# Performance work log

Hardware: AMD Instinct MI355X
Metric: run time of the kernel (lower is better)

## Reference

```python
import jax, jax.numpy as jnp
import numpy as np

NEG_SLOPE = 0.2  # leaky_relu_negative_slope


def setup_inputs() -> dict:
    key = jax.random.key(0)
    k = jax.random.split(key, 6)
    N = 1024          # n_nodes == nei_nodes (forced by the asserts in forward)
    IN = 256          # in_features
    OUT = 256         # out_features (nei_embedding feature dim, since linear_r = Linear(out_features, ...))
    H, F = 4, 64      # n_heads, n_hidden = out_features // n_heads
    h = jax.random.normal(k[0], (N, IN), dtype=jnp.float32)
    nei_embedding = jax.random.normal(k[1], (N, OUT), dtype=jnp.float32)
    adj_mat = jax.random.randint(k[2], (N, N), 0, 2).astype(jnp.float32)
    scale = 0.05
    w_l = jax.random.normal(k[3], (IN, H * F), dtype=jnp.float32) * scale   # linear_l.weight.T
    w_r = jax.random.normal(k[4], (OUT, H * F), dtype=jnp.float32) * scale  # linear_r.weight.T
    attn_w = jax.random.normal(k[5], (F,), dtype=jnp.float32) * scale       # attn.weight (1, F) -> (F,)
    return {"h": h, "nei_embedding": nei_embedding, "adj_mat": adj_mat,
            "w_l": w_l, "w_r": w_r, "attn_w": attn_w, "use_elu": 1}


def reference(h, nei_embedding, adj_mat, w_l, w_r, attn_w, use_elu):
    N = h.shape[0]
    M = nei_embedding.shape[0]
    F = attn_w.shape[0]
    H = w_l.shape[1] // F
    g_l = (h @ w_l).reshape(N, H, F)              # (N, H, F)
    g_r = (nei_embedding @ w_r).reshape(M, H, F)  # (M, H, F)
    # Torch does repeat/repeat_interleave then view(n, m, H, F); with the
    # assert-enforced n == m this is exactly g_sum[i, j] = g_l[j] + g_r[i].
    g_sum = g_r[:, None, :, :] + g_l[None, :, :, :]          # (N, N, H, F)
    e = jnp.einsum("nmhf,f->nmh", jax.nn.leaky_relu(g_sum, NEG_SLOPE), attn_w)
    adj_t = adj_mat.T[:, :, None]                             # (M, N, 1) -> broadcasts over heads
    e = jnp.where(adj_t == 0, -jnp.inf, e)
    exp_attention = jnp.exp(e)
    weighted = exp_attention * adj_t                          # (N, N, H)
    denom = jnp.sum(weighted, axis=1, keepdims=True)
    a = weighted / denom                                      # masked softmax over neighbors
    # dropout is identity at inference
    attn_res = jnp.einsum("ijh,jhf->ihf", a, g_r)            # (N, H, F)
    if use_elu:
        attn_res = jax.nn.elu(attn_res)
    return attn_res.reshape(N, H * F)  # is_concat=True
```

## Files before the change

### kernel.cpp

```cpp
#include <hip/hip_runtime.h>
#include <math.h>

#define NN 1024
#define KK 256
#define NH 4
#define FD 64
#define HF 256

__global__ __launch_bounds__(256) void gatv2_gemm(
    const float* __restrict__ h, const float* __restrict__ nei,
    const float* __restrict__ w_l, const float* __restrict__ w_r,
    float* __restrict__ g_l, float* __restrict__ g_r)
{
    const float* A; const float* W; float* G;
    if (blockIdx.z == 0) { A = h;   W = w_l; G = g_l; }
    else                 { A = nei; W = w_r; G = g_r; }

    __shared__ float sA[16][68];
    __shared__ float sW[16][64];

    const int t   = threadIdx.x;
    const int tm4 = (t >> 4) << 2;
    const int tn4 = (t & 15) << 2;
    const int m0  = blockIdx.y * 64;
    const int n0  = blockIdx.x * 64;

    float acc[4][4] = {};

    const int ar = t >> 2, ac = (t & 3) << 2;
    const int wr = t >> 4, wc = (t & 15) << 2;

    for (int k0 = 0; k0 < KK; k0 += 16) {
        float4 va = *(const float4*)&A[(size_t)(m0 + ar)*KK + k0 + ac];
        float4 vw = *(const float4*)&W[(size_t)(k0 + wr)*HF + n0 + wc];
        __syncthreads();
        sA[ac+0][ar] = va.x; sA[ac+1][ar] = va.y;
        sA[ac+2][ar] = va.z; sA[ac+3][ar] = va.w;
        *(float4*)&sW[wr][wc] = vw;
        __syncthreads();
        #pragma unroll
        for (int kk = 0; kk < 16; ++kk) {
            float4 a4 = *(const float4*)&sA[kk][tm4];
            float4 w4 = *(const float4*)&sW[kk][tn4];
            const float am[4] = {a4.x, a4.y, a4.z, a4.w};
            const float wn[4] = {w4.x, w4.y, w4.z, w4.w};
            #pragma unroll
            for (int mi = 0; mi < 4; ++mi)
                #pragma unroll
                for (int ni = 0; ni < 4; ++ni)
                    acc[mi][ni] += am[mi] * wn[ni];
        }
    }
    #pragma unroll
    for (int mi = 0; mi < 4; ++mi)
        *(float4*)&G[(size_t)(m0 + tm4 + mi)*HF + n0 + tn4] =
            make_float4(acc[mi][0], acc[mi][1], acc[mi][2], acc[mi][3]);
}

__global__ __launch_bounds__(256) void gatv2_cl(
    const float* __restrict__ g_l, const float* __restrict__ aw, float* __restrict__ cl)
{
    const int idx = blockIdx.x*256 + threadIdx.x;
    const int j = idx >> 2, hh = idx & 3;
    const float4* row = (const float4*)(g_l + (size_t)j*HF + hh*FD);
    const float4* wp  = (const float4*)aw;
    float s = 0.f;
    #pragma unroll
    for (int q = 0; q < 16; ++q) {
        float4 g = row[q], w = wp[q];
        s += g.x*w.x + g.y*w.y + g.z*w.z + g.w*w.w;
    }
    cl[idx] = 0.6f * s;
}

__global__ __launch_bounds__(256, 2) void gatv2_attn(
    const float* __restrict__ g_l, const float* __restrict__ g_r,
    const float* __restrict__ adj, const float* __restrict__ attn_w,
    const float* __restrict__ cl,
    float* __restrict__ accP, float* __restrict__ denP, int JPB)
{
    const int t  = threadIdx.x;
    const int jc = blockIdx.x;
    const int ib = blockIdx.y;
    const int hh = blockIdx.z;
    const int i  = ib*256 + t;

    const float4* wp = (const float4*)attn_w;

    float4 gri[16];
    float crdot = 0.f;
    {
        const float4* gp = (const float4*)(g_r + (size_t)i*HF + hh*FD);
        #pragma unroll
        for (int q = 0; q < 16; ++q) {
            float4 g = gp[q], w = wp[q];
            gri[q] = g;
            crdot += w.x*g.x + w.y*g.y + w.z*g.z + w.w*g.w;
        }
    }
    const float cr = 0.6f * crdot;

    float4 acc[16];
    #pragma unroll
    for (int q = 0; q < 16; ++q) acc[q] = make_float4(0.f,0.f,0.f,0.f);
    float denom = 0.f;

    const int jbase = jc * JPB;
    const float* glh = g_l + (size_t)hh*FD;
    const float* grh = g_r + (size_t)hh*FD;

    float mask_next = adj[(size_t)jbase*NN + i];
    for (int jj = 0; jj < JPB; ++jj) {
        const int j = jbase + jj;
        const float mask = mask_next;
        if (jj + 1 < JPB) mask_next = adj[(size_t)(j + 1)*NN + i];
        const float clj = cl[j*NH + hh];
        const float4* glr = (const float4*)(glh + (size_t)j*HF);
        float e0 = 0.f, e1 = 0.f, e2 = 0.f, e3 = 0.f;
        #pragma unroll
        for (int q = 0; q < 16; ++q) {
            float4 g = glr[q], w = wp[q];
            e0 += w.x * fabsf(g.x + gri[q].x);
            e1 += w.y * fabsf(g.y + gri[q].y);
            e2 += w.z * fabsf(g.z + gri[q].z);
            e3 += w.w * fabsf(g.w + gri[q].w);
        }
        const float e = cr + clj + 0.4f * ((e0+e1) + (e2+e3));
        const float pw = (mask != 0.f) ? __expf(e) : 0.f;
        denom += pw;
        const float4* grr = (const float4*)(grh + (size_t)j*HF);
        #pragma unroll
        for (int q = 0; q < 16; ++q) {
            float4 g = grr[q];
            acc[q].x += pw*g.x; acc[q].y += pw*g.y;
            acc[q].z += pw*g.z; acc[q].w += pw*g.w;
        }
    }
    float* op = accP + (size_t)jc*(NN*HF) + ((size_t)i*NH + hh)*FD;
    #pragma unroll
    for (int q = 0; q < 16; ++q) ((float4*)op)[q] = acc[q];
    denP[(size_t)jc*(NN*NH) + (size_t)i*NH + hh] = denom;
}

__global__ __launch_bounds__(256) void gatv2_reduce(
    const float* __restrict__ accP, const float* __restrict__ denP,
    const int* __restrict__ use_elu, float* __restrict__ out, int NC)
{
    const int idx = blockIdx.x*256 + threadIdx.x;
    float s = 0.f, d = 0.f;
    for (int c = 0; c < NC; ++c) {
        s += accP[(size_t)c*(NN*HF) + idx];
        d += denP[(size_t)c*(NN*NH) + (idx >> 6)];
    }
    float r = s / d;
    if (*use_elu != 0) r = (r > 0.f) ? r : expm1f(r);
    out[idx] = r;
}

extern "C" void kernel_launch(void* const* d_in, const int* in_sizes, int n_in,
                              void* d_out, int out_size, void* d_ws, size_t ws_size,
                              hipStream_t stream)
{
    const float* h    = (const float*)d_in[0];
    const float* nei  = (const float*)d_in[1];
    const float* adj  = (const float*)d_in[2];
    const float* w_l  = (const float*)d_in[3];
    const float* w_r  = (const float*)d_in[4];
    const float* aw   = (const float*)d_in[5];
    const int*   uel  = (const int*)d_in[6];
    float* out = (float*)d_out;
    float* ws  = (float*)d_ws;

    float* g_l = ws;
    float* g_r = g_l + (size_t)NN*HF;
    float* cl  = g_r + (size_t)NN*HF;

    int NC = 32;
    while (NC > 1) {
        size_t need = ((size_t)2*NN*HF + (size_t)NN*NH
                     + (size_t)NC*NN*NH + (size_t)NC*NN*HF) * sizeof(float);
        if (need <= ws_size) break;
        NC >>= 1;
    }
    const int JPB = NN / NC;

    float* denP = cl + (size_t)NN*NH;
    float* accP = denP + (size_t)NC*NN*NH;

    hipLaunchKernelGGL(gatv2_gemm, dim3(HF/64, NN/64, 2), dim3(256), 0, stream,
                       h, nei, w_l, w_r, g_l, g_r);
    hipLaunchKernelGGL(gatv2_cl, dim3((NN*NH)/256), dim3(256), 0, stream,
                       g_l, aw, cl);
    hipLaunchKernelGGL(gatv2_attn, dim3(NC, NN/256, NH), dim3(256), 0, stream,
                       g_l, g_r, adj, aw, cl, accP, denP, JPB);
    hipLaunchKernelGGL(gatv2_reduce, dim3((NN*HF)/256), dim3(256), 0, stream,
                       accP, denP, uel, out, NC);
}
```

Baseline: 171.0 us.

## Split attention into score kernel with scalar loads and separate PV kernel

Replaces the single fused attention kernel with a score kernel that writes the full masked exp matrix P to workspace, and a separate P·g_r accumulation kernel. The score kernel loads wave-uniform g_l rows through scalar loads in inline asm. The GEMM now computes the cl/cr attention dot products in its epilogue with atomics, which removes the separate cl kernel. Denominators are accumulated atomically after a memset. The aim is to cut redundant vector loads and register pressure in the attention loop, at the cost of a 16MB intermediate P round-trip through memory, an extra memset, and float atomics that make summation order nondeterministic.

```diff
diff --git a/kernel.cpp b/kernel.cpp
--- a/kernel.cpp
+++ b/kernel.cpp
@@ -7,152 +7,206 @@
 #define FD 64
 #define HF 256
 
+typedef __attribute__((ext_vector_type(16))) float fx16;
+
+#define OFF_GL   0
+#define OFF_GR   (256*1024)
+#define OFF_CL   (512*1024)
+#define OFF_CR   (512*1024 + 4096)
+#define OFF_DEN  (512*1024 + 8192)
+#define OFF_P    (512*1024 + 12288)
+#define OFF_ACCP (OFF_P + 4*1024*1024)
+
 __global__ __launch_bounds__(256) void gatv2_gemm(
-    const float* __restrict__ h, const float* __restrict__ nei,
+    const float* __restrict__ hmat, const float* __restrict__ nei,
     const float* __restrict__ w_l, const float* __restrict__ w_r,
-    float* __restrict__ g_l, float* __restrict__ g_r)
-{
-    const float* A; const float* W; float* G;
-    if (blockIdx.z == 0) { A = h;   W = w_l; G = g_l; }
-    else                 { A = nei; W = w_r; G = g_r; }
-
-    __shared__ float sA[16][68];
-    __shared__ float sW[16][64];
-
-    const int t   = threadIdx.x;
-    const int tm4 = (t >> 4) << 2;
-    const int tn4 = (t & 15) << 2;
-    const int m0  = blockIdx.y * 64;
-    const int n0  = blockIdx.x * 64;
-
-    float acc[4][4] = {};
-
-    const int ar = t >> 2, ac = (t & 3) << 2;
-    const int wr = t >> 4, wc = (t & 15) << 2;
-
-    for (int k0 = 0; k0 < KK; k0 += 16) {
-        float4 va = *(const float4*)&A[(size_t)(m0 + ar)*KK + k0 + ac];
-        float4 vw = *(const float4*)&W[(size_t)(k0 + wr)*HF + n0 + wc];
-        __syncthreads();
-        sA[ac+0][ar] = va.x; sA[ac+1][ar] = va.y;
-        sA[ac+2][ar] = va.z; sA[ac+3][ar] = va.w;
-        *(float4*)&sW[wr][wc] = vw;
-        __syncthreads();
+    const float* __restrict__ aw, float* __restrict__ ws)
+{
+    __shared__ float sA[64*257];
+    const int t  = threadIdx.x;
+    const int mb = blockIdx.x;
+    const int hh = blockIdx.y;
+    const int mat = blockIdx.z;
+    const float* A = mat ? nei : hmat;
+    const float* W = mat ? w_r : w_l;
+    float* G  = ws + (mat ? OFF_GR : OFF_GL);
+    float* CC = ws + (mat ? OFF_CR : OFF_CL);
+
+    const int lane = t & 63;
+    const int wv   = t >> 6;
+    const int m    = mb*64 + lane;
+    const int n0   = hh*64 + wv*16;
+
+    #pragma unroll
+    for (int rep = 0; rep < 16; ++rep) {
+        const int flat = rep*1024 + t*4;
+        const int r = flat >> 8, c = flat & 255;
+        *(float4*)&sA[r*257 + c] = *(const float4*)&A[(size_t)(mb*64 + r)*KK + c];
+    }
+    __syncthreads();
+
+    float acc[16] = {};
+    const float* wp = W + n0;
+    #pragma unroll 4
+    for (int k = 0; k < KK; ++k) {
+        const float a = sA[lane*257 + k];
+        const float4 w0 = *(const float4*)(wp + (size_t)k*HF);
+        const float4 w1 = *(const float4*)(wp + (size_t)k*HF + 4);
+        const float4 w2 = *(const float4*)(wp + (size_t)k*HF + 8);
+        const float4 w3 = *(const float4*)(wp + (size_t)k*HF + 12);
+        acc[0]  += a*w0.x; acc[1]  += a*w0.y; acc[2]  += a*w0.z; acc[3]  += a*w0.w;
+        acc[4]  += a*w1.x; acc[5]  += a*w1.y; acc[6]  += a*w1.z; acc[7]  += a*w1.w;
+        acc[8]  += a*w2.x; acc[9]  += a*w2.y; acc[10] += a*w2.z; acc[11] += a*w2.w;
+        acc[12] += a*w3.x; acc[13] += a*w3.y; acc[14] += a*w3.z; acc[15] += a*w3.w;
+    }
+
+    {
+        const float4* awp = (const float4*)(aw + wv*16);
+        float wd = 0.f;
         #pragma unroll
-        for (int kk = 0; kk < 16; ++kk) {
-            float4 a4 = *(const float4*)&sA[kk][tm4];
-            float4 w4 = *(const float4*)&sW[kk][tn4];
-            const float am[4] = {a4.x, a4.y, a4.z, a4.w};
-            const float wn[4] = {w4.x, w4.y, w4.z, w4.w};
-            #pragma unroll
-            for (int mi = 0; mi < 4; ++mi)
-                #pragma unroll
-                for (int ni = 0; ni < 4; ++ni)
-                    acc[mi][ni] += am[mi] * wn[ni];
+        for (int c = 0; c < 4; ++c) {
+            const float4 w4 = awp[c];
+            wd += w4.x*acc[c*4] + w4.y*acc[c*4+1] + w4.z*acc[c*4+2] + w4.w*acc[c*4+3];
         }
-    }
-    #pragma unroll
-    for (int mi = 0; mi < 4; ++mi)
-        *(float4*)&G[(size_t)(m0 + tm4 + mi)*HF + n0 + tn4] =
-            make_float4(acc[mi][0], acc[mi][1], acc[mi][2], acc[mi][3]);
-}
-
-__global__ __launch_bounds__(256) void gatv2_cl(
-    const float* __restrict__ g_l, const float* __restrict__ aw, float* __restrict__ cl)
-{
-    const int idx = blockIdx.x*256 + threadIdx.x;
-    const int j = idx >> 2, hh = idx & 3;
-    const float4* row = (const float4*)(g_l + (size_t)j*HF + hh*FD);
-    const float4* wp  = (const float4*)aw;
-    float s = 0.f;
-    #pragma unroll
-    for (int q = 0; q < 16; ++q) {
-        float4 g = row[q], w = wp[q];
-        s += g.x*w.x + g.y*w.y + g.z*w.z + g.w*w.w;
-    }
-    cl[idx] = 0.6f * s;
-}
-
-__global__ __launch_bounds__(256, 2) void gatv2_attn(
-    const float* __restrict__ g_l, const float* __restrict__ g_r,
-    const float* __restrict__ adj, const float* __restrict__ attn_w,
-    const float* __restrict__ cl,
-    float* __restrict__ accP, float* __restrict__ denP, int JPB)
-{
+        atomicAdd(&CC[hh*NN + m], 0.6f*wd);
+    }
+
+    __syncthreads();
+    #pragma unroll
+    for (int c = 0; c < 4; ++c)
+        *(float4*)&sA[lane*65 + wv*16 + c*4] =
+            make_float4(acc[c*4], acc[c*4+1], acc[c*4+2], acc[c*4+3]);
+    __syncthreads();
+    #pragma unroll
+    for (int rep = 0; rep < 4; ++rep) {
+        const int flat = rep*1024 + t*4;
+        const int ml = flat >> 6, f = flat & 63;
+        const float4 v = *(const float4*)&sA[ml*65 + f];
+        *(float4*)&G[(size_t)(mb*64 + ml)*HF + hh*64 + f] = v;
+    }
+}
+
+#define EBLK(RV, QB)                                              \
+    { _Pragma("unroll") for (int q = 0; q < 4; ++q) {             \
+        const float4 wq = w[(QB)+q]; const float4 gq = gri[(QB)+q]; \
+        e0 += wq.x * fabsf(RV[q*4+0] + gq.x);                     \
+        e1 += wq.y * fabsf(RV[q*4+1] + gq.y);                     \
+        e2 += wq.z * fabsf(RV[q*4+2] + gq.z);                     \
+        e3 += wq.w * fabsf(RV[q*4+3] + gq.w); } }
+
+__global__ __launch_bounds__(256, 3) void gatv2_e(
+    const float* __restrict__ wsro, const float* __restrict__ adj,
+    const float* __restrict__ aw, float* __restrict__ P,
+    float* __restrict__ den)
+{
+    const float* g_l = wsro + OFF_GL;
+    const float* g_r = wsro + OFF_GR;
+    const float* cl  = wsro + OFF_CL;
+    const float* cr  = wsro + OFF_CR;
     const int t  = threadIdx.x;
     const int jc = blockIdx.x;
     const int ib = blockIdx.y;
     const int hh = blockIdx.z;
     const int i  = ib*256 + t;
 
-    const float4* wp = (const float4*)attn_w;
-
-    float4 gri[16];
-    float crdot = 0.f;
+    float4 w[16], gri[16];
     {
-        const float4* gp = (const float4*)(g_r + (size_t)i*HF + hh*FD);
+        const float4* awp = (const float4*)aw;
+        const float4* gp  = (const float4*)(g_r + (size_t)i*HF + hh*FD);
         #pragma unroll
-        for (int q = 0; q < 16; ++q) {
-            float4 g = gp[q], w = wp[q];
-            gri[q] = g;
-            crdot += w.x*g.x + w.y*g.y + w.z*g.z + w.w*g.w;
-        }
-    }
-    const float cr = 0.6f * crdot;
-
-    float4 acc[16];
-    #pragma unroll
-    for (int q = 0; q < 16; ++q) acc[q] = make_float4(0.f,0.f,0.f,0.f);
-    float denom = 0.f;
-
-    const int jbase = jc * JPB;
-    const float* glh = g_l + (size_t)hh*FD;
-    const float* grh = g_r + (size_t)hh*FD;
-
-    float mask_next = adj[(size_t)jbase*NN + i];
+        for (int q = 0; q < 16; ++q) { w[q] = awp[q]; gri[q] = gp[q]; }
+    }
+    const float cri = cr[hh*NN + i];
+
+    float denl = 0.f;
+    const int j0 = jc*32;
+    for (int jj = 0; jj < 32; ++jj) {
+        const int j = j0 + jj;
+        const float mask = adj[(size_t)j*NN + i];
+        fx16 r0, r1, r2, r3; float clv;
+        const float* rowp = g_l + (size_t)j*HF + hh*FD;
+        const float* clp  = cl + hh*NN + j;
+        asm volatile(
+            "s_load_dwordx16 %0, %5, 0x0\n\t"
+            "s_load_dwordx16 %1, %5, 0x40\n\t"
+            "s_load_dwordx16 %2, %5, 0x80\n\t"
+            "s_load_dwordx16 %3, %5, 0xc0\n\t"
+            "s_load_dword %4, %6, 0x0\n\t"
+            "s_waitcnt lgkmcnt(0)"
+            : "=s"(r0), "=s"(r1), "=s"(r2), "=s"(r3), "=s"(clv)
+            : "s"(rowp), "s"(clp));
+        float e0 = 0.f, e1 = 0.f, e2 = 0.f, e3 = 0.f;
+        EBLK(r0, 0) EBLK(r1, 4) EBLK(r2, 8) EBLK(r3, 12)
+        const float e  = cri + clv + 0.4f*((e0+e1)+(e2+e3));
+        const float pw = (mask != 0.f) ? __expf(e) : 0.f;
+        denl += pw;
+        P[((size_t)hh*NN + j)*NN + i] = pw;
+    }
+    atomicAdd(&den[hh*NN + i], denl);
+}
+
+__global__ __launch_bounds__(256) void gatv2_pv(
+    const float* __restrict__ wsro, float* __restrict__ accP, int JC2)
+{
+    __shared__ float sT[128*65];
+    const float* g_r = wsro + OFF_GR;
+    const float* P   = wsro + OFF_P;
+    const int t  = threadIdx.x;
+    const int jc = blockIdx.x;
+    const int ib = blockIdx.y;
+    const int hh = blockIdx.z;
+    const int wv = t >> 6, l = t & 63;
+    const int i1 = ib*128 + l;
+    const int f0 = hh*FD + wv*16;
+    const int JPB = NN / JC2;
+
+    float4 a1[4] = {}, a2[4] = {};
+    const int j0 = jc*JPB;
+    #pragma unroll 2
     for (int jj = 0; jj < JPB; ++jj) {
-        const int j = jbase + jj;
-        const float mask = mask_next;
-        if (jj + 1 < JPB) mask_next = adj[(size_t)(j + 1)*NN + i];
-        const float clj = cl[j*NH + hh];
-        const float4* glr = (const float4*)(glh + (size_t)j*HF);
-        float e0 = 0.f, e1 = 0.f, e2 = 0.f, e3 = 0.f;
-        #pragma unroll
-        for (int q = 0; q < 16; ++q) {
-            float4 g = glr[q], w = wp[q];
-            e0 += w.x * fabsf(g.x + gri[q].x);
-            e1 += w.y * fabsf(g.y + gri[q].y);
-            e2 += w.z * fabsf(g.z + gri[q].z);
-            e3 += w.w * fabsf(g.w + gri[q].w);
-        }
-        const float e = cr + clj + 0.4f * ((e0+e1) + (e2+e3));
-        const float pw = (mask != 0.f) ? __expf(e) : 0.f;
-        denom += pw;
-        const float4* grr = (const float4*)(grh + (size_t)j*HF);
-        #pragma unroll
-        for (int q = 0; q < 16; ++q) {
-            float4 g = grr[q];
-            acc[q].x += pw*g.x; acc[q].y += pw*g.y;
-            acc[q].z += pw*g.z; acc[q].w += pw*g.w;
-        }
-    }
-    float* op = accP + (size_t)jc*(NN*HF) + ((size_t)i*NH + hh)*FD;
-    #pragma unroll
-    for (int q = 0; q < 16; ++q) ((float4*)op)[q] = acc[q];
-    denP[(size_t)jc*(NN*NH) + (size_t)i*NH + hh] = denom;
-}
-
-__global__ __launch_bounds__(256) void gatv2_reduce(
-    const float* __restrict__ accP, const float* __restrict__ denP,
-    const int* __restrict__ use_elu, float* __restrict__ out, int NC)
+        const int j = j0 + jj;
+        const float* rp = g_r + (size_t)j*HF + f0;
+        const float4 r0 = ((const float4*)rp)[0];
+        const float4 r1 = ((const float4*)rp)[1];
+        const float4 r2 = ((const float4*)rp)[2];
+        const float4 r3 = ((const float4*)rp)[3];
+        const size_t pbase = ((size_t)hh*NN + j)*NN + i1;
+        const float p1 = P[pbase];
+        const float p2 = P[pbase + 64];
+        a1[0].x += p1*r0.x; a1[0].y += p1*r0.y; a1[0].z += p1*r0.z; a1[0].w += p1*r0.w;
+        a1[1].x += p1*r1.x; a1[1].y += p1*r1.y; a1[1].z += p1*r1.z; a1[1].w += p1*r1.w;
+        a1[2].x += p1*r2.x; a1[2].y += p1*r2.y; a1[2].z += p1*r2.z; a1[2].w += p1*r2.w;
+        a1[3].x += p1*r3.x; a1[3].y += p1*r3.y; a1[3].z += p1*r3.z; a1[3].w += p1*r3.w;
+        a2[0].x += p2*r0.x; a2[0].y += p2*r0.y; a2[0].z += p2*r0.z; a2[0].w += p2*r0.w;
+        a2[1].x += p2*r1.x; a2[1].y += p2*r1.y; a2[1].z += p2*r1.z; a2[1].w += p2*r1.w;
+        a2[2].x += p2*r2.x; a2[2].y += p2*r2.y; a2[2].z += p2*r2.z; a2[2].w += p2*r2.w;
+        a2[3].x += p2*r3.x; a2[3].y += p2*r3.y; a2[3].z += p2*r3.z; a2[3].w += p2*r3.w;
+    }
+
+    #pragma unroll
+    for (int c = 0; c < 4; ++c) {
+        *(float4*)&sT[(l     )*65 + wv*16 + c*4] = a1[c];
+        *(float4*)&sT[(l + 64)*65 + wv*16 + c*4] = a2[c];
+    }
+    __syncthreads();
+    #pragma unroll
+    for (int rep = 0; rep < 8; ++rep) {
+        const int flat = rep*1024 + t*4;
+        const int il = flat >> 6, f = flat & 63;
+        const float4 v = *(const float4*)&sT[il*65 + f];
+        *(float4*)&accP[(size_t)jc*(NN*HF) + (size_t)(ib*128 + il)*HF + hh*64 + f] = v;
+    }
+}
+
+__global__ __launch_bounds__(256) void gatv2_fin(
+    const float* __restrict__ accP, const float* __restrict__ den,
+    const int* __restrict__ use_elu, float* __restrict__ out, int JC2)
 {
     const int idx = blockIdx.x*256 + threadIdx.x;
-    float s = 0.f, d = 0.f;
-    for (int c = 0; c < NC; ++c) {
-        s += accP[(size_t)c*(NN*HF) + idx];
-        d += denP[(size_t)c*(NN*NH) + (idx >> 6)];
-    }
-    float r = s / d;
+    const int i = idx >> 8, hh = (idx >> 6) & 3;
+    float s = 0.f;
+    for (int c = 0; c < JC2; ++c) s += accP[(size_t)c*(NN*HF) + idx];
+    float r = s / den[hh*NN + i];
     if (*use_elu != 0) r = (r > 0.f) ? r : expm1f(r);
     out[idx] = r;
 }
@@ -161,7 +215,7 @@
                               void* d_out, int out_size, void* d_ws, size_t ws_size,
                               hipStream_t stream)
 {
-    const float* h    = (const float*)d_in[0];
+    const float* hmat = (const float*)d_in[0];
     const float* nei  = (const float*)d_in[1];
     const float* adj  = (const float*)d_in[2];
     const float* w_l  = (const float*)d_in[3];
@@ -171,28 +225,17 @@
     float* out = (float*)d_out;
     float* ws  = (float*)d_ws;
 
-    float* g_l = ws;
-    float* g_r = g_l + (size_t)NN*HF;
-    float* cl  = g_r + (size_t)NN*HF;
-
-    int NC = 32;
-    while (NC > 1) {
-        size_t need = ((size_t)2*NN*HF + (size_t)NN*NH
-                     + (size_t)NC*NN*NH + (size_t)NC*NN*HF) * sizeof(float);
-        if (need <= ws_size) break;
-        NC >>= 1;
-    }
-    const int JPB = NN / NC;
-
-    float* denP = cl + (size_t)NN*NH;
-    float* accP = denP + (size_t)NC*NN*NH;
-
-    hipLaunchKernelGGL(gatv2_gemm, dim3(HF/64, NN/64, 2), dim3(256), 0, stream,
-                       h, nei, w_l, w_r, g_l, g_r);
-    hipLaunchKernelGGL(gatv2_cl, dim3((NN*NH)/256), dim3(256), 0, stream,
-                       g_l, aw, cl);
-    hipLaunchKernelGGL(gatv2_attn, dim3(NC, NN/256, NH), dim3(256), 0, stream,
-                       g_l, g_r, adj, aw, cl, accP, denP, JPB);
-    hipLaunchKernelGGL(gatv2_reduce, dim3((NN*HF)/256), dim3(256), 0, stream,
-                       accP, denP, uel, out, NC);
-}
+    int JC2 = 16;
+    if (((size_t)OFF_ACCP + (size_t)16*NN*HF) * 4 > ws_size) JC2 = 8;
+
+    hipMemsetAsync((void*)(ws + OFF_CL), 0, 3*4096*sizeof(float), stream);
+
+    hipLaunchKernelGGL(gatv2_gemm, dim3(16,4,2), dim3(256), 0, stream,
+                       hmat, nei, w_l, w_r, aw, ws);
+    hipLaunchKernelGGL(gatv2_e, dim3(32,4,4), dim3(256), 0, stream,
+                       ws, adj, aw, ws + OFF_P, ws + OFF_DEN);
+    hipLaunchKernelGGL(gatv2_pv, dim3(JC2,8,4), dim3(256), 0, stream,
+                       ws, ws + OFF_ACCP, JC2);
+    hipLaunchKernelGGL(gatv2_fin, dim3((NN*HF)/256), dim3(256), 0, stream,
+                       ws + OFF_ACCP, ws + OFF_DEN, uel, out, JC2);
+}
```

After: 181.5 us. +6.2%, slower.
